# Kernel optimization log

Hardware: AMD Instinct MI355X
Metric: run time of the kernel (lower is better)

Reference implementation:

```python
import jax, jax.numpy as jnp
import numpy as np

N_NODES = 10000
IN_CH = 512
HID = 128
HEADS = 4
OUT_CH = 256
N_EDGES = 160000
NEG_SLOPE = 0.2  # PyG GATConv default


def gat_conv(x, src, dst, W, a_src, a_dst, b):
    """PyG-style GATConv. x:[N,F_in], W:[F_in,H*C], a_src/a_dst:[H,C], b:[H*C].
    src/dst already include self-loops. Returns [N, H*C] (concat heads)."""
    N = x.shape[0]
    H, C = a_src.shape
    h = (x @ W).reshape(N, H, C)                     # [N,H,C]
    e_src = jnp.einsum('nhc,hc->nh', h, a_src)        # [N,H]
    e_dst = jnp.einsum('nhc,hc->nh', h, a_dst)
    alpha = jax.nn.leaky_relu(e_src[src] + e_dst[dst], NEG_SLOPE)  # [E,H]
    # softmax over incoming edges of each destination node
    m = jax.ops.segment_max(alpha, dst, num_segments=N)            # [N,H]
    ex = jnp.exp(alpha - m[dst])
    denom = jax.ops.segment_sum(ex, dst, num_segments=N)           # [N,H]
    coeff = ex / (denom[dst] + 1e-16)                              # [E,H]
    out = jax.ops.segment_sum(coeff[:, :, None] * h[src], dst, num_segments=N)  # [N,H,C]
    return out.reshape(N, H * C) + b


def _edges_with_self_loops(edge_index, n):
    loops = jnp.arange(n, dtype=edge_index.dtype)
    src = jnp.concatenate([edge_index[0], loops])
    dst = jnp.concatenate([edge_index[1], loops])
    return src, dst


def setup_inputs() -> dict:
    key = jax.random.key(0)
    ks = jax.random.split(key, 20)
    s = 0.05
    inp = {
        'x': jax.random.normal(ks[0], (N_NODES, IN_CH), jnp.float32),
        'W1': jax.random.normal(ks[1], (IN_CH, HEADS * HID), jnp.float32) * s,
        'a1s': jax.random.normal(ks[2], (HEADS, HID), jnp.float32) * s,
        'a1d': jax.random.normal(ks[3], (HEADS, HID), jnp.float32) * s,
        'b1': jnp.zeros((HEADS * HID,), jnp.float32),
        'W2': jax.random.normal(ks[4], (HEADS * HID, HEADS * HID), jnp.float32) * s,
        'a2s': jax.random.normal(ks[5], (HEADS, HID), jnp.float32) * s,
        'a2d': jax.random.normal(ks[6], (HEADS, HID), jnp.float32) * s,
        'b2': jnp.zeros((HEADS * HID,), jnp.float32),
        'W3': jax.random.normal(ks[7], (HEADS * HID, HID), jnp.float32) * s,
        'a3s': jax.random.normal(ks[8], (1, HID), jnp.float32) * s,
        'a3d': jax.random.normal(ks[9], (1, HID), jnp.float32) * s,
        'b3': jnp.zeros((HID,), jnp.float32),
        'Wl': jax.random.normal(ks[10], (HID, OUT_CH), jnp.float32) * s,
        'bl': jnp.zeros((OUT_CH,), jnp.float32),
        'Wr': jax.random.normal(ks[11], (IN_CH, OUT_CH), jnp.float32) * s,
        'br': jnp.zeros((OUT_CH,), jnp.float32),
        'edge_index': jax.random.randint(ks[12], (2, N_EDGES), 0, N_NODES, jnp.int64 if jax.config.jax_enable_x64 else jnp.int32),
    }
    return inp


def reference(x, W1, a1s, a1d, b1, W2, a2s, a2d, b2, W3, a3s, a3d, b3, Wl, bl, Wr, br, edge_index):
    src, dst = _edges_with_self_loops(edge_index, x.shape[0])
    residual = x @ Wr + br
    h = jax.nn.elu(gat_conv(x, src, dst, W1, a1s, a1d, b1))
    h = jax.nn.elu(gat_conv(h, src, dst, W2, a2s, a2d, b2))
    h = jax.nn.elu(gat_conv(h, src, dst, W3, a3s, a3d, b3))
    return h @ Wl + bl + residual
```

## Files before the change

kernel.cpp:

```cpp
#include <hip/hip_runtime.h>
#include <hip/hip_bf16.h>
#include <cstdint>
#include <cstddef>

#define N_NODES 10000
#define M_PAD   10240
#define HEADS   4

typedef __bf16 bfrag8 __attribute__((ext_vector_type(8)));
typedef __bf16 bfrag2 __attribute__((ext_vector_type(2)));
typedef float  floatx4 __attribute__((ext_vector_type(4)));
typedef float  floatx2 __attribute__((ext_vector_type(2)));

#define S0V (M_PAD * 512 / 8)
#define S1E (512 * 512 / 8)
#define S2E (512 * 512 / 8)
#define S3E (512 * 128 / 8)
#define S4E (128 * 256 / 8)
#define S5E (512 * 256 / 8)

__global__ __launch_bounds__(256) void prep(const float* __restrict__ x,
                                            const float* __restrict__ W1,
                                            const float* __restrict__ W2,
                                            const float* __restrict__ W3,
                                            const float* __restrict__ Wl,
                                            const float* __restrict__ Wr,
                                            const int* __restrict__ edst, int E,
                                            __bf16* __restrict__ xb,
                                            __bf16* __restrict__ W1T,
                                            __bf16* __restrict__ W2T,
                                            __bf16* __restrict__ W3T,
                                            __bf16* __restrict__ WlT,
                                            __bf16* __restrict__ WrT,
                                            int* __restrict__ deg) {
    int i = blockIdx.x * 256 + threadIdx.x;
    if (i < S0V) {
        int base = i * 8;
        int row = base >> 9;
        bfrag8 r = {};
        if (row < N_NODES) {
            float4 f0 = ((const float4*)x)[i * 2];
            float4 f1 = ((const float4*)x)[i * 2 + 1];
            r[0] = (__bf16)f0.x; r[1] = (__bf16)f0.y; r[2] = (__bf16)f0.z; r[3] = (__bf16)f0.w;
            r[4] = (__bf16)f1.x; r[5] = (__bf16)f1.y; r[6] = (__bf16)f1.z; r[7] = (__bf16)f1.w;
        }
        *(bfrag8*)(xb + base) = r;
    } else if ((i -= S0V) < S1E) {
        int n = i & 511, kb = (i >> 9) * 8;
        bfrag8 r;
#pragma unroll
        for (int t = 0; t < 8; ++t) r[t] = (__bf16)W1[(kb + t) * 512 + n];
        *(bfrag8*)(W1T + n * 512 + kb) = r;
    } else if ((i -= S1E) < S2E) {
        int n = i & 511, kb = (i >> 9) * 8;
        bfrag8 r;
#pragma unroll
        for (int t = 0; t < 8; ++t) r[t] = (__bf16)W2[(kb + t) * 512 + n];
        *(bfrag8*)(W2T + n * 512 + kb) = r;
    } else if ((i -= S2E) < S3E) {
        int n = i & 127, kb = (i >> 7) * 8;
        bfrag8 r;
#pragma unroll
        for (int t = 0; t < 8; ++t) r[t] = (__bf16)W3[(kb + t) * 128 + n];
        *(bfrag8*)(W3T + n * 512 + kb) = r;
    } else if ((i -= S3E) < S4E) {
        int n = i & 255, kb = (i >> 8) * 8;
        bfrag8 r;
#pragma unroll
        for (int t = 0; t < 8; ++t) r[t] = (__bf16)Wl[(kb + t) * 256 + n];
        *(bfrag8*)(WlT + n * 128 + kb) = r;
    } else if ((i -= S4E) < S5E) {
        int n = i & 255, kb = (i >> 8) * 8;
        bfrag8 r;
#pragma unroll
        for (int t = 0; t < 8; ++t) r[t] = (__bf16)Wr[(kb + t) * 256 + n];
        *(bfrag8*)(WrT + n * 512 + kb) = r;
    } else if ((i -= S5E) < E) {
        atomicAdd(&deg[edst[i]], 1);
    }
}


__global__ __launch_bounds__(256) void scan_kernel(const int* __restrict__ deg,
                                                   int* __restrict__ rowptr,
                                                   int* __restrict__ cursor, int n) {
    __shared__ int wtot[4], woff[4];
    int t = threadIdx.x, lane = t & 63, wv = t >> 6;
    int chunk = (n + 255) / 256;
    int beg = t * chunk, end = beg + chunk; if (end > n) end = n; if (beg > n) beg = n;
    int s = 0;
    for (int i = beg; i < end; ++i) s += deg[i] + 1;
    int v = s;
#pragma unroll
    for (int off = 1; off < 64; off <<= 1) {
        int o = __shfl_up(v, off);
        if (lane >= off) v += o;
    }
    if (lane == 63) wtot[wv] = v;
    __syncthreads();
    if (t == 0) {
        int r = 0;
#pragma unroll
        for (int i = 0; i < 4; ++i) { woff[i] = r; r += wtot[i]; }
        rowptr[n] = r;
    }
    __syncthreads();
    int off = woff[wv] + v - s;
    for (int i = beg; i < end; ++i) {
        rowptr[i] = off; cursor[i] = off;
        off += deg[i] + 1;
    }
}

__global__ __launch_bounds__(256) void scatter_kernel(const int* __restrict__ src,
                                                      const int* __restrict__ dst, int E, int n,
                                                      int* __restrict__ cursor,
                                                      int* __restrict__ csr) {
    int i = blockIdx.x * 256 + threadIdx.x;
    if (i < E) {
        int pos = atomicAdd(&cursor[dst[i]], 1);
        csr[pos] = src[i];
    } else if (i < E + n) {
        int v = i - E;
        int pos = atomicAdd(&cursor[v], 1);
        csr[pos] = v;
    }
}


template <int NT>
__device__ __forceinline__ void gemm_loop(const __bf16* __restrict__ A,
                                          const __bf16* __restrict__ BT, int K,
                                          int m0, int n0, int wave, int lane,
                                          __bf16* As, __bf16* Bs,
                                          floatx4 (&acc)[2][NT]) {
    int r = wave * 8 + (lane >> 3);
    int kof = (lane & 7) * 8;
    const __bf16* gA = A + (size_t)(m0 + r) * K + kof;
    const __bf16* gB = BT + (size_t)(n0 + r) * K + kof;
    __bf16* lA = As + r * 64 + kof;
    __bf16* lB = Bs + r * 64 + kof;
    const __bf16* fA = As + (wave * 32 + (lane & 15)) * 64 + (lane >> 4) * 8;
    const __bf16* fB = Bs + (lane & 15) * 64 + (lane >> 4) * 8;

    for (int k0 = 0; k0 < K; k0 += 64) {
#pragma unroll
        for (int u = 0; u < 4; ++u)
            __builtin_amdgcn_global_load_lds(
                (const __attribute__((address_space(1))) void*)(gA + (size_t)u * 32 * K),
                (__attribute__((address_space(3))) void*)(lA + u * 32 * 64), 16, 0, 0);
#pragma unroll
        for (int u = 0; u < NT / 2; ++u)
            __builtin_amdgcn_global_load_lds(
                (const __attribute__((address_space(1))) void*)(gB + (size_t)u * 32 * K),
                (__attribute__((address_space(3))) void*)(lB + u * 32 * 64), 16, 0, 0);
        gA += 64; gB += 64;
        __syncthreads();

#pragma unroll
        for (int ks = 0; ks < 2; ++ks) {
            bfrag8 a0 = *(const bfrag8*)(fA + ks * 32);
            bfrag8 a1 = *(const bfrag8*)(fA + 16 * 64 + ks * 32);
#pragma unroll
            for (int nt = 0; nt < NT; ++nt) {
                bfrag8 b = *(const bfrag8*)(fB + nt * 16 * 64 + ks * 32);
                acc[0][nt] = __builtin_amdgcn_mfma_f32_16x16x32_bf16(a0, b, acc[0][nt], 0, 0, 0);
                acc[1][nt] = __builtin_amdgcn_mfma_f32_16x16x32_bf16(a1, b, acc[1][nt], 0, 0, 0);
            }
        }
        __syncthreads();
    }
}

__global__ __launch_bounds__(256) void gemm_h(const __bf16* __restrict__ A,
                                              const __bf16* __restrict__ BT,
                                              unsigned char* __restrict__ C8,
                                              int N, int K, int H,
                                              const float* __restrict__ as_,
                                              const float* __restrict__ ad_,
                                              float* __restrict__ esp,
                                              float* __restrict__ edp) {
    __shared__ __align__(16) __bf16 As[128 * 64];
    __shared__ __align__(16) __bf16 Bs[128 * 64];
    int tid = threadIdx.x, wave = tid >> 6, lane = tid & 63;
    int m0 = blockIdx.x * 128, n0 = blockIdx.y * 128;
    floatx4 acc[2][8] = {};
    gemm_loop<8>(A, BT, K, m0, n0, wave, lane, As, Bs, acc);

    int crow = m0 + wave * 32 + (lane >> 4) * 4;
    int ccol = n0 + (lane & 15);
#pragma unroll
    for (int mt = 0; mt < 2; ++mt)
#pragma unroll
        for (int nt = 0; nt < 8; ++nt)
#pragma unroll
            for (int r = 0; r < 4; ++r) {
                float v = acc[mt][nt][r];
                size_t o = (size_t)(crow + mt * 16 + r) * N + ccol + nt * 16;
                int p = __builtin_amdgcn_cvt_pk_fp8_f32(v, v, 0, false);
                C8[o] = (unsigned char)(p & 0xff);
            }

    int head = n0 >> 7;
    float a_sv[8], a_dv[8];
#pragma unroll
    for (int nt = 0; nt < 8; ++nt) {
        int cin = nt * 16 + (lane & 15);
        a_sv[nt] = as_[head * 128 + cin];
        a_dv[nt] = ad_[head * 128 + cin];
    }
#pragma unroll
    for (int mt = 0; mt < 2; ++mt)
#pragma unroll
        for (int r = 0; r < 4; ++r) {
            float ps = 0.f, pd = 0.f;
#pragma unroll
            for (int nt = 0; nt < 8; ++nt) {
                float v = acc[mt][nt][r];
                ps += v * a_sv[nt];
                pd += v * a_dv[nt];
            }
#pragma unroll
            for (int off = 8; off; off >>= 1) {
                ps += __shfl_xor(ps, off);
                pd += __shfl_xor(pd, off);
            }
            if ((lane & 15) == 0) {
                int row = crow + mt * 16 + r;
                esp[row * H + head] = ps;
                edp[row * H + head] = pd;
            }
        }
}

__global__ __launch_bounds__(256) void gemm_final(const __bf16* __restrict__ A1,
                                                  const __bf16* __restrict__ B1T, int K1,
                                                  const __bf16* __restrict__ A2,
                                                  const __bf16* __restrict__ B2T, int K2,
                                                  float* __restrict__ C,
                                                  const float* __restrict__ bias1,
                                                  const float* __restrict__ bias2,
                                                  int M, int N) {
    __shared__ __align__(16) __bf16 As[128 * 64];
    __shared__ __align__(16) __bf16 Bs[64 * 64];
    int tid = threadIdx.x, wave = tid >> 6, lane = tid & 63;
    int m0 = blockIdx.x * 128, n0 = blockIdx.y * 64;
    floatx4 acc[2][4] = {};
    gemm_loop<4>(A1, B1T, K1, m0, n0, wave, lane, As, Bs, acc);
    gemm_loop<4>(A2, B2T, K2, m0, n0, wave, lane, As, Bs, acc);

    int crow = m0 + wave * 32 + (lane >> 4) * 4;
    int ccol = n0 + (lane & 15);
#pragma unroll
    for (int mt = 0; mt < 2; ++mt)
#pragma unroll
        for (int nt = 0; nt < 4; ++nt)
#pragma unroll
            for (int r = 0; r < 4; ++r) {
                int row = crow + mt * 16 + r;
                int col = ccol + nt * 16;
                if (row < M)
                    C[(size_t)row * N + col] = acc[mt][nt][r] + bias1[col] + bias2[col];
            }
}


template <int H>
__global__ __launch_bounds__(256) void gather_agg(const unsigned char* __restrict__ H8,
                                                  const float* __restrict__ esp,
                                                  const float* __restrict__ edp,
                                                  const int* __restrict__ rowptr,
                                                  const int* __restrict__ csr,
                                                  const float* __restrict__ bias,
                                                  __bf16* __restrict__ outb) {
    constexpr int F = H * 128;
    constexpr int CH = F / 64;
    int wave = threadIdx.x >> 6, lane = threadIdx.x & 63;
    int node = blockIdx.x * 4 + wave;
    if (node >= M_PAD) return;
    int hsel = (H == 4) ? (lane >> 4) : 0;
    __bf16* op = outb + (size_t)node * F + lane * CH;
    if (node >= N_NODES) {
        if (H == 4) { bfrag8 z = {}; *(bfrag8*)op = z; }
        else        { bfrag2 z = {}; *(bfrag2*)op = z; }
        return;
    }
    const unsigned char* hp = H8 + lane * CH;
    float edv = edp[node * H + hsel];
    int beg = rowptr[node], end = rowptr[node + 1];
    float acc[CH] = {};
    float wsum = 0.f;
    int j = beg;
    for (; j + 7 < end; j += 8) {
        int s[8];
        float e[8];
#pragma unroll
        for (int u = 0; u < 8; ++u) s[u] = csr[j + u];
#pragma unroll
        for (int u = 0; u < 8; ++u)
            e[u] = esp[s[u] * H + hsel];
        if (H == 4) {
            uint2 p[8];
#pragma unroll
            for (int u = 0; u < 8; ++u) p[u] = *(const uint2*)(hp + (size_t)s[u] * F);
#pragma unroll
            for (int u = 0; u < 8; ++u) {
                float t = e[u] + edv;
                t = t > 0.f ? t : 0.2f * t;
                float wgt = __expf(t);
                wsum += wgt;
                floatx2 f0 = __builtin_amdgcn_cvt_pk_f32_fp8(p[u].x, false);
                floatx2 f1 = __builtin_amdgcn_cvt_pk_f32_fp8(p[u].x, true);
                floatx2 f2 = __builtin_amdgcn_cvt_pk_f32_fp8(p[u].y, false);
                floatx2 f3 = __builtin_amdgcn_cvt_pk_f32_fp8(p[u].y, true);
                acc[0] += wgt * f0[0]; acc[1] += wgt * f0[1];
                acc[2] += wgt * f1[0]; acc[3] += wgt * f1[1];
                acc[4] += wgt * f2[0]; acc[5] += wgt * f2[1];
                acc[6] += wgt * f3[0]; acc[7] += wgt * f3[1];
            }
        } else {
            unsigned short p[8];
#pragma unroll
            for (int u = 0; u < 8; ++u) p[u] = *(const unsigned short*)(hp + (size_t)s[u] * F);
#pragma unroll
            for (int u = 0; u < 8; ++u) {
                float t = e[u] + edv;
                t = t > 0.f ? t : 0.2f * t;
                float wgt = __expf(t);
                wsum += wgt;
                floatx2 f0 = __builtin_amdgcn_cvt_pk_f32_fp8((int)p[u], false);
                acc[0] += wgt * f0[0]; acc[1] += wgt * f0[1];
            }
        }
    }
    for (; j < end; ++j) {
        int s0 = csr[j];
        float t = esp[s0 * H + hsel] + edv;
        t = t > 0.f ? t : 0.2f * t;
        float wgt = __expf(t);
        wsum += wgt;
        if (H == 4) {
            uint2 p = *(const uint2*)(hp + (size_t)s0 * F);
            floatx2 f0 = __builtin_amdgcn_cvt_pk_f32_fp8(p.x, false);
            floatx2 f1 = __builtin_amdgcn_cvt_pk_f32_fp8(p.x, true);
            floatx2 f2 = __builtin_amdgcn_cvt_pk_f32_fp8(p.y, false);
            floatx2 f3 = __builtin_amdgcn_cvt_pk_f32_fp8(p.y, true);
            acc[0] += wgt * f0[0]; acc[1] += wgt * f0[1];
            acc[2] += wgt * f1[0]; acc[3] += wgt * f1[1];
            acc[4] += wgt * f2[0]; acc[5] += wgt * f2[1];
            acc[6] += wgt * f3[0]; acc[7] += wgt * f3[1];
        } else {
            unsigned short p = *(const unsigned short*)(hp + (size_t)s0 * F);
            floatx2 f0 = __builtin_amdgcn_cvt_pk_f32_fp8((int)p, false);
            acc[0] += wgt * f0[0]; acc[1] += wgt * f0[1];
        }
    }
    float inv = 1.f / (wsum + 1e-16f);
    if (H == 4) {
        bfrag8 r;
#pragma unroll
        for (int k = 0; k < 8; ++k) {
            float o = acc[k] * inv + bias[lane * 8 + k];
            o = o > 0.f ? o : __expf(o) - 1.f;
            r[k] = (__bf16)o;
        }
        *(bfrag8*)op = r;
    } else {
        bfrag2 r;
#pragma unroll
        for (int k = 0; k < 2; ++k) {
            float o = acc[k] * inv + bias[lane * 2 + k];
            o = o > 0.f ? o : __expf(o) - 1.f;
            r[k] = (__bf16)o;
        }
        *(bfrag2*)op = r;
    }
}


extern "C" void kernel_launch(void* const* d_in, const int* in_sizes, int n_in,
                              void* d_out, int out_size, void* d_ws, size_t ws_size,
                              hipStream_t stream) {
    const float* x   = (const float*)d_in[0];
    const float* W1  = (const float*)d_in[1];
    const float* a1s = (const float*)d_in[2];
    const float* a1d = (const float*)d_in[3];
    const float* b1  = (const float*)d_in[4];
    const float* W2  = (const float*)d_in[5];
    const float* a2s = (const float*)d_in[6];
    const float* a2d = (const float*)d_in[7];
    const float* b2  = (const float*)d_in[8];
    const float* W3  = (const float*)d_in[9];
    const float* a3s = (const float*)d_in[10];
    const float* a3d = (const float*)d_in[11];
    const float* b3  = (const float*)d_in[12];
    const float* Wl  = (const float*)d_in[13];
    const float* bl  = (const float*)d_in[14];
    const float* Wr  = (const float*)d_in[15];
    const float* br  = (const float*)d_in[16];
    const int*   ei  = (const int*)d_in[17];
    const int E = in_sizes[17] / 2;
    const int* esrc = ei;
    const int* edst = ei + E;
    const int slots = E + N_NODES;
    float* out = (float*)d_out;

    char* w = (char*)d_ws;
    auto alloc = [&](size_t b) { char* p = w; w += (b + 255) & ~(size_t)255; return p; };
    __bf16* xb  = (__bf16*)alloc((size_t)M_PAD * 512 * 2);
    __bf16* hb  = (__bf16*)alloc((size_t)M_PAD * 512 * 2);
    __bf16* hb3 = (__bf16*)alloc((size_t)M_PAD * 128 * 2);
    unsigned char* Hi8 = (unsigned char*)alloc((size_t)M_PAD * 512);
    __bf16* W1T = (__bf16*)alloc(512 * 512 * 2);
    __bf16* W2T = (__bf16*)alloc(512 * 512 * 2);
    __bf16* W3T = (__bf16*)alloc(128 * 512 * 2);
    __bf16* WlT = (__bf16*)alloc(256 * 128 * 2);
    __bf16* WrT = (__bf16*)alloc(256 * 512 * 2);
    float* esp    = (float*)alloc((size_t)M_PAD * HEADS * 4);
    float* edp    = (float*)alloc((size_t)M_PAD * HEADS * 4);
    int*   deg    = (int*)alloc(N_NODES * 4);
    int*   rowptr = (int*)alloc((N_NODES + 1) * 4);
    int*   cursor = (int*)alloc(N_NODES * 4);
    int*   csr    = (int*)alloc((size_t)slots * 4);

    (void)hipMemsetAsync(deg, 0, N_NODES * sizeof(int), stream);

    const int sp_total = S0V + S1E + S2E + S3E + S4E + S5E + E;
    prep<<<(sp_total + 255) / 256, 256, 0, stream>>>(x, W1, W2, W3, Wl, Wr, edst, E,
                                                     xb, W1T, W2T, W3T, WlT, WrT, deg);
    scan_kernel<<<1, 256, 0, stream>>>(deg, rowptr, cursor, N_NODES);
    scatter_kernel<<<(E + N_NODES + 255) / 256, 256, 0, stream>>>(esrc, edst, E, N_NODES,
                                                                  cursor, csr);

    gemm_h<<<dim3(M_PAD / 128, 4), 256, 0, stream>>>(xb, W1T, Hi8, 512, 512, 4,
                                                     a1s, a1d, esp, edp);
    gather_agg<4><<<M_PAD / 4, 256, 0, stream>>>(Hi8, esp, edp, rowptr, csr, b1, hb);
    gemm_h<<<dim3(M_PAD / 128, 4), 256, 0, stream>>>(hb, W2T, Hi8, 512, 512, 4,
                                                     a2s, a2d, esp, edp);
    gather_agg<4><<<M_PAD / 4, 256, 0, stream>>>(Hi8, esp, edp, rowptr, csr, b2, hb);
    gemm_h<<<dim3(M_PAD / 128, 1), 256, 0, stream>>>(hb, W3T, Hi8, 128, 512, 1,
                                                     a3s, a3d, esp, edp);
    gather_agg<1><<<M_PAD / 4, 256, 0, stream>>>(Hi8, esp, edp, rowptr, csr, b3, hb3);
    gemm_final<<<dim3(M_PAD / 128, 4), 256, 0, stream>>>(xb, WrT, 512, hb3, WlT, 128,
                                                         out, br, bl, N_NODES, 256);
}
```

Baseline: 263.9 us.

## Precompute per-edge attention weights cooperatively in LDS and widen scan block

Result: faster. 243.5 us (-7.7%).

```diff
diff --git a/kernel.cpp b/kernel.cpp
--- a/kernel.cpp
+++ b/kernel.cpp
@@ -81,12 +81,12 @@
 }
 
 
-__global__ __launch_bounds__(256) void scan_kernel(const int* __restrict__ deg,
-                                                   int* __restrict__ rowptr,
-                                                   int* __restrict__ cursor, int n) {
-    __shared__ int wtot[4], woff[4];
+__global__ __launch_bounds__(1024) void scan_kernel(const int* __restrict__ deg,
+                                                    int* __restrict__ rowptr,
+                                                    int* __restrict__ cursor, int n) {
+    __shared__ int wtot[16], woff[16];
     int t = threadIdx.x, lane = t & 63, wv = t >> 6;
-    int chunk = (n + 255) / 256;
+    int chunk = (n + 1023) / 1024;
     int beg = t * chunk, end = beg + chunk; if (end > n) end = n; if (beg > n) beg = n;
     int s = 0;
     for (int i = beg; i < end; ++i) s += deg[i] + 1;
@@ -101,7 +101,7 @@
     if (t == 0) {
         int r = 0;
 #pragma unroll
-        for (int i = 0; i < 4; ++i) { woff[i] = r; r += wtot[i]; }
+        for (int i = 0; i < 16; ++i) { woff[i] = r; r += wtot[i]; }
         rowptr[n] = r;
     }
     __syncthreads();
@@ -275,86 +275,111 @@
                                                   __bf16* __restrict__ outb) {
     constexpr int F = H * 128;
     constexpr int CH = F / 64;
+    __shared__ int   sIdx[4][64];
+    __shared__ float sWgt[4][64 * H];
     int wave = threadIdx.x >> 6, lane = threadIdx.x & 63;
     int node = blockIdx.x * 4 + wave;
     if (node >= M_PAD) return;
-    int hsel = (H == 4) ? (lane >> 4) : 0;
     __bf16* op = outb + (size_t)node * F + lane * CH;
     if (node >= N_NODES) {
         if (H == 4) { bfrag8 z = {}; *(bfrag8*)op = z; }
         else        { bfrag2 z = {}; *(bfrag2*)op = z; }
         return;
     }
+    int hsel = (H == 4) ? (lane >> 4) : 0;
     const unsigned char* hp = H8 + lane * CH;
-    float edv = edp[node * H + hsel];
     int beg = rowptr[node], end = rowptr[node + 1];
     float acc[CH] = {};
     float wsum = 0.f;
-    int j = beg;
-    for (; j + 7 < end; j += 8) {
-        int s[8];
-        float e[8];
-#pragma unroll
-        for (int u = 0; u < 8; ++u) s[u] = csr[j + u];
-#pragma unroll
-        for (int u = 0; u < 8; ++u)
-            e[u] = esp[s[u] * H + hsel];
-        if (H == 4) {
-            uint2 p[8];
-#pragma unroll
-            for (int u = 0; u < 8; ++u) p[u] = *(const uint2*)(hp + (size_t)s[u] * F);
-#pragma unroll
-            for (int u = 0; u < 8; ++u) {
-                float t = e[u] + edv;
-                t = t > 0.f ? t : 0.2f * t;
-                float wgt = __expf(t);
-                wsum += wgt;
-                floatx2 f0 = __builtin_amdgcn_cvt_pk_f32_fp8(p[u].x, false);
-                floatx2 f1 = __builtin_amdgcn_cvt_pk_f32_fp8(p[u].x, true);
-                floatx2 f2 = __builtin_amdgcn_cvt_pk_f32_fp8(p[u].y, false);
-                floatx2 f3 = __builtin_amdgcn_cvt_pk_f32_fp8(p[u].y, true);
+
+    float edv0 = 0.f, edv1 = 0.f, edv2 = 0.f, edv3 = 0.f;
+    if (H == 4) {
+        float4 e4 = *(const float4*)(edp + node * 4);
+        edv0 = e4.x; edv1 = e4.y; edv2 = e4.z; edv3 = e4.w;
+    } else {
+        edv0 = edp[node];
+    }
+
+    for (int t0 = beg; t0 < end; t0 += 64) {
+        int n_t = end - t0; if (n_t > 64) n_t = 64;
+        if (lane < n_t) {
+            int s = csr[t0 + lane];
+            sIdx[wave][lane] = s;
+            if (H == 4) {
+                float4 es = *(const float4*)(esp + s * 4);
+                float tt0 = es.x + edv0; tt0 = tt0 > 0.f ? tt0 : 0.2f * tt0;
+                float tt1 = es.y + edv1; tt1 = tt1 > 0.f ? tt1 : 0.2f * tt1;
+                float tt2 = es.z + edv2; tt2 = tt2 > 0.f ? tt2 : 0.2f * tt2;
+                float tt3 = es.w + edv3; tt3 = tt3 > 0.f ? tt3 : 0.2f * tt3;
+                floatx4 w4 = { __expf(tt0), __expf(tt1), __expf(tt2), __expf(tt3) };
+                *(floatx4*)&sWgt[wave][lane * 4] = w4;
+            } else {
+                float tt = esp[s] + edv0; tt = tt > 0.f ? tt : 0.2f * tt;
+                sWgt[wave][lane] = __expf(tt);
+            }
+        }
+        asm volatile("s_waitcnt lgkmcnt(0)" ::: "memory");
+
+        int e = 0;
+        for (; e + 3 < n_t; e += 4) {
+            int s4[4]; float w4[4];
+#pragma unroll
+            for (int u = 0; u < 4; ++u) {
+                s4[u] = sIdx[wave][e + u];
+                w4[u] = sWgt[wave][(e + u) * H + hsel];
+            }
+            if (H == 4) {
+                uint2 p4[4];
+#pragma unroll
+                for (int u = 0; u < 4; ++u) p4[u] = *(const uint2*)(hp + (size_t)s4[u] * F);
+#pragma unroll
+                for (int u = 0; u < 4; ++u) {
+                    float wgt = w4[u];
+                    wsum += wgt;
+                    floatx2 f0 = __builtin_amdgcn_cvt_pk_f32_fp8(p4[u].x, false);
+                    floatx2 f1 = __builtin_amdgcn_cvt_pk_f32_fp8(p4[u].x, true);
+                    floatx2 f2 = __builtin_amdgcn_cvt_pk_f32_fp8(p4[u].y, false);
+                    floatx2 f3 = __builtin_amdgcn_cvt_pk_f32_fp8(p4[u].y, true);
+                    acc[0] += wgt * f0[0]; acc[1] += wgt * f0[1];
+                    acc[2] += wgt * f1[0]; acc[3] += wgt * f1[1];
+                    acc[4] += wgt * f2[0]; acc[5] += wgt * f2[1];
+                    acc[6] += wgt * f3[0]; acc[7] += wgt * f3[1];
+                }
+            } else {
+                unsigned short p4[4];
+#pragma unroll
+                for (int u = 0; u < 4; ++u) p4[u] = *(const unsigned short*)(hp + (size_t)s4[u] * F);
+#pragma unroll
+                for (int u = 0; u < 4; ++u) {
+                    float wgt = w4[u];
+                    wsum += wgt;
+                    floatx2 f0 = __builtin_amdgcn_cvt_pk_f32_fp8((int)p4[u], false);
+                    acc[0] += wgt * f0[0]; acc[1] += wgt * f0[1];
+                }
+            }
+        }
+        for (; e < n_t; ++e) {
+            int s0 = sIdx[wave][e];
+            float wgt = sWgt[wave][e * H + hsel];
+            wsum += wgt;
+            if (H == 4) {
+                uint2 p = *(const uint2*)(hp + (size_t)s0 * F);
+                floatx2 f0 = __builtin_amdgcn_cvt_pk_f32_fp8(p.x, false);
+                floatx2 f1 = __builtin_amdgcn_cvt_pk_f32_fp8(p.x, true);
+                floatx2 f2 = __builtin_amdgcn_cvt_pk_f32_fp8(p.y, false);
+                floatx2 f3 = __builtin_amdgcn_cvt_pk_f32_fp8(p.y, true);
                 acc[0] += wgt * f0[0]; acc[1] += wgt * f0[1];
                 acc[2] += wgt * f1[0]; acc[3] += wgt * f1[1];
                 acc[4] += wgt * f2[0]; acc[5] += wgt * f2[1];
                 acc[6] += wgt * f3[0]; acc[7] += wgt * f3[1];
-            }
-        } else {
-            unsigned short p[8];
-#pragma unroll
-            for (int u = 0; u < 8; ++u) p[u] = *(const unsigned short*)(hp + (size_t)s[u] * F);
-#pragma unroll
-            for (int u = 0; u < 8; ++u) {
-                float t = e[u] + edv;
-                t = t > 0.f ? t : 0.2f * t;
-                float wgt = __expf(t);
-                wsum += wgt;
-                floatx2 f0 = __builtin_amdgcn_cvt_pk_f32_fp8((int)p[u], false);
+            } else {
+                unsigned short p = *(const unsigned short*)(hp + (size_t)s0 * F);
+                floatx2 f0 = __builtin_amdgcn_cvt_pk_f32_fp8((int)p, false);
                 acc[0] += wgt * f0[0]; acc[1] += wgt * f0[1];
             }
         }
     }
-    for (; j < end; ++j) {
-        int s0 = csr[j];
-        float t = esp[s0 * H + hsel] + edv;
-        t = t > 0.f ? t : 0.2f * t;
-        float wgt = __expf(t);
-        wsum += wgt;
-        if (H == 4) {
-            uint2 p = *(const uint2*)(hp + (size_t)s0 * F);
-            floatx2 f0 = __builtin_amdgcn_cvt_pk_f32_fp8(p.x, false);
-            floatx2 f1 = __builtin_amdgcn_cvt_pk_f32_fp8(p.x, true);
-            floatx2 f2 = __builtin_amdgcn_cvt_pk_f32_fp8(p.y, false);
-            floatx2 f3 = __builtin_amdgcn_cvt_pk_f32_fp8(p.y, true);
-            acc[0] += wgt * f0[0]; acc[1] += wgt * f0[1];
-            acc[2] += wgt * f1[0]; acc[3] += wgt * f1[1];
-            acc[4] += wgt * f2[0]; acc[5] += wgt * f2[1];
-            acc[6] += wgt * f3[0]; acc[7] += wgt * f3[1];
-        } else {
-            unsigned short p = *(const unsigned short*)(hp + (size_t)s0 * F);
-            floatx2 f0 = __builtin_amdgcn_cvt_pk_f32_fp8((int)p, false);
-            acc[0] += wgt * f0[0]; acc[1] += wgt * f0[1];
-        }
-    }
+
     float inv = 1.f / (wsum + 1e-16f);
     if (H == 4) {
         bfrag8 r;
@@ -428,7 +453,7 @@
     const int sp_total = S0V + S1E + S2E + S3E + S4E + S5E + E;
     prep<<<(sp_total + 255) / 256, 256, 0, stream>>>(x, W1, W2, W3, Wl, Wr, edst, E,
                                                      xb, W1T, W2T, W3T, WlT, WrT, deg);
-    scan_kernel<<<1, 256, 0, stream>>>(deg, rowptr, cursor, N_NODES);
+    scan_kernel<<<1, 1024, 0, stream>>>(deg, rowptr, cursor, N_NODES);
     scatter_kernel<<<(E + N_NODES + 255) / 256, 256, 0, stream>>>(esrc, edst, E, N_NODES,
                                                                   cursor, csr);
 
```
